# Optimization experiments

Measured on AMD Instinct MI355X. Metric: run time of the kernel, lower is better.

Reference implementation:

```python
import jax, jax.numpy as jnp
import numpy as np

B, T, N, D = 32, 12, 325, 64
H = 4           # geo_num_heads == t_num_heads
HD = D // H     # head_dim = 16
M_SP = 32       # spatial frequency modes (min(32, N//2))
M_T = T // 2    # temporal frequency modes (all low modes)
SCALE = HD ** -0.5


def _lin(x, W):
    # torch nn.Linear (no bias): y = x @ W.T, W: [out, in]
    return jnp.einsum('btnd,ed->btne', x, W)


def _spatial(x, Wq, Wk, Wv, weights_Q, sp_modes):
    # FEDformer-style frequency attention over the node axis N
    q, k, v = _lin(x, Wq), _lin(x, Wk), _lin(x, Wv)          # [B,T,N,D]
    prep = lambda y: y.reshape(B, T, N, H, HD).transpose(0, 1, 3, 4, 2)  # [B,T,H,HD,N]
    qn = prep(q) / jnp.linalg.norm(q)   # global Frobenius norm (torch.norm with no dim)
    kn = prep(k) / jnp.linalg.norm(k)
    vn = prep(v)
    # rfft over nodes, gather selected modes (scatter-into-zeros in torch == gather here
    # since target indices are 0..M-1)
    qf = jnp.fft.rfft(qn, axis=-1)[..., sp_modes]            # [B,T,H,HD,M] c64
    kf = jnp.fft.rfft(kn, axis=-1)[..., sp_modes]
    vf = jnp.fft.rfft(vn, axis=-1)[..., sp_modes]
    M = M_SP
    qg = qf.transpose(0, 1, 2, 4, 3)[:, :, :, :, None, :]    # [B,T,H,M,1,HD]
    wq = jnp.broadcast_to(weights_Q.astype(jnp.complex64), (B, T, H, M, M - 1, HD))
    q_cat = jnp.concatenate([qg, wq], axis=4)                # [B,T,H,M,M,HD]
    kg = kf.transpose(0, 1, 2, 4, 3)[:, :, :, None, :, :]    # [B,T,H,1,M,HD]
    att = kg * jnp.conj(q_cat) * SCALE                       # [B,T,H,M,M,HD] c64
    att = jax.nn.softmax(jnp.abs(att), axis=-2).astype(jnp.complex64)
    att = att.transpose(0, 1, 2, 3, 5, 4)                    # [B,T,H,M,HD,M]
    vg = vf[:, :, :, None, :, :]                             # [B,T,H,1,HD,M]
    out = (vg * jnp.conj(att)).mean(axis=3)                  # [B,T,H,HD,M]
    out_ft = jnp.zeros((B, T, H, HD, N // 2 + 1), jnp.complex64).at[..., sp_modes].set(out)
    y = jnp.fft.irfft(out_ft, n=N, axis=-1)                  # [B,T,H,HD,N]
    return y.transpose(0, 1, 4, 2, 3).reshape(B, T, N, D)


def _temporal(x, Wq, Wk, Wv, weights_Q_t, t_modes):
    # frequency attention over the time axis T with causal (tril) mask.
    # NOTE: torch reshapes the [B,T,N,D] buffer directly as [B,N,T,H,HD] (raw view),
    # so we replicate that exact buffer reinterpretation.
    q, k, v = _lin(x, Wq), _lin(x, Wk), _lin(x, Wv)
    prep = lambda y: y.reshape(B, N, T, H, HD).transpose(0, 1, 3, 4, 2)  # [B,N,H,HD,T]
    qn = prep(q); kn = prep(k); vn = prep(v)
    qn = qn / jnp.linalg.norm(qn)
    kn = kn / jnp.linalg.norm(kn)
    qf = jnp.fft.rfft(qn, axis=-1)[..., t_modes]             # [B,N,H,HD,Mt]
    kf = jnp.fft.rfft(kn, axis=-1)[..., t_modes]
    vf = jnp.fft.rfft(vn, axis=-1)[..., t_modes]
    Mt = M_T
    qg = qf.transpose(0, 1, 2, 4, 3)[:, :, :, :, None, :]    # [B,N,H,Mt,1,HD]
    wq = jnp.broadcast_to(weights_Q_t.astype(jnp.complex64), (B, N, H, Mt, Mt - 1, HD))
    q_cat = jnp.concatenate([qg, wq], axis=4)                # [B,N,H,Mt,Mt,HD]
    kg = kf.transpose(0, 1, 2, 4, 3)[:, :, :, :, None, :]    # [B,N,H,Mt,1,HD] (unsqueeze(4) in torch)
    att = kg * jnp.conj(q_cat) * SCALE                       # [B,N,H,Mt,Mt,HD]
    att = att.transpose(0, 1, 2, 5, 3, 4)                    # [B,N,H,HD,Mt,Mt]
    mask = jnp.tril(jnp.ones((Mt, Mt), jnp.float32))
    att = att * mask                                         # zero above diagonal
    attw = jax.nn.softmax(jnp.abs(att), axis=-1).astype(jnp.complex64)
    vg = vf[..., None]                                       # [B,N,H,HD,Mt,1]
    out = (vg * jnp.conj(attw)).mean(axis=-1)                # [B,N,H,HD,Mt]
    out_ft = jnp.zeros((B, N, H, HD, T // 2 + 1), jnp.complex64).at[..., t_modes].set(out)
    y = jnp.fft.irfft(out_ft, n=T, axis=-1)                  # [B,N,H,HD,T]
    return y.transpose(0, 4, 1, 2, 3).reshape(B, T, N, D)


def _gcn(x, adj, W_fc1, W_mlp, b_mlp):
    a = adj / jnp.sum(adj, axis=1, keepdims=True)            # row-normalized
    agg = jnp.einsum('btkd,nk->btnd', x, a)
    h = jnp.einsum('btnd,ed->btne', agg, W_fc1)              # fc1 (no bias)
    return jnp.einsum('btnd,ed->btne', h, W_mlp) + b_mlp     # mlp (bias)


def _forward(x, adj, Wq_geo, Wk_geo, Wv_geo, Wq_t, Wk_t, Wv_t,
             W_fc1, W_mlp, b_mlp, weights_Q, weights_Q_t, sp_modes, t_modes):
    gcn_out = _gcn(x, adj, W_fc1, W_mlp, b_mlp)
    sp_x = _spatial(x, Wq_geo, Wk_geo, Wv_geo, weights_Q, sp_modes)
    te_x = _temporal(x, Wq_t, Wk_t, Wv_t, weights_Q_t, t_modes)
    return gcn_out + sp_x + te_x   # proj_drop is identity (p=0)


def setup_inputs() -> dict:
    key = jax.random.key(0)
    ks = jax.random.split(key, 13)
    w = lambda k, s: jax.random.normal(k, s, dtype=jnp.float32) * 0.05
    rng = np.random.default_rng(0)
    sp_modes = np.sort(rng.permutation(N // 2)[:M_SP]).astype(np.int32)
    t_modes = np.arange(M_T, dtype=np.int32)  # modes_T == T//2 selects all low modes
    return {
        'x': jax.random.normal(ks[0], (B, T, N, D), dtype=jnp.float32),
        'adj': jax.random.uniform(ks[1], (N, N), dtype=jnp.float32),
        'Wq_geo': w(ks[2], (D, D)), 'Wk_geo': w(ks[3], (D, D)), 'Wv_geo': w(ks[4], (D, D)),
        'Wq_t': w(ks[5], (D, D)), 'Wk_t': w(ks[6], (D, D)), 'Wv_t': w(ks[7], (D, D)),
        'W_fc1': w(ks[8], (D, D)), 'W_mlp': w(ks[9], (D, D)), 'b_mlp': w(ks[10], (D,)),
        'weights_Q': jax.random.normal(ks[11], (M_SP, M_SP - 1, HD), dtype=jnp.float32),
        'weights_Q_t': jax.random.normal(ks[12], (M_T, M_T - 1, HD), dtype=jnp.float32),
        'sp_modes': jnp.asarray(sp_modes),
        't_modes': jnp.asarray(t_modes),
    }


def reference(x, adj, Wq_geo, Wk_geo, Wv_geo, Wq_t, Wk_t, Wv_t,
              W_fc1, W_mlp, b_mlp, weights_Q, weights_Q_t, sp_modes, t_modes):
    return _forward(x, adj, Wq_geo, Wk_geo, Wv_geo, Wq_t, Wk_t, Wv_t,
                    W_fc1, W_mlp, b_mlp, weights_Q, weights_Q_t, sp_modes, t_modes)
```

## Files before the change

kernel.cpp:

```cpp
#include <hip/hip_runtime.h>


typedef unsigned short u16;
typedef short short8 __attribute__((ext_vector_type(8)));
typedef float floatx4 __attribute__((ext_vector_type(4)));

__device__ __forceinline__ u16 f2bf(float f) {
  union { float fp; unsigned int u; } v; v.fp = f;
  unsigned int x = v.u;
  x += 0x7FFF + ((x >> 16) & 1);
  return (u16)(x >> 16);
}

constexpr size_t OFF_NPART = 4096;
constexpr size_t OFF_WQA  = 8208;
constexpr size_t OFF_ANB  = 24080;
constexpr size_t OFF_TB   = 81280;
constexpr size_t OFF_WVTB = 92544;
constexpr size_t OFF_WBB  = 94592;
constexpr size_t OFF_T2   = 102080;
constexpr size_t OFF_OFT  = 112480;
constexpr size_t OFF_XCT  = 898912;
constexpr size_t OFF_XA   = 13211488;
constexpr size_t OFF_WSPB = OFF_XA + 8192;

__global__ __launch_bounds__(256) void k_prep(const float* __restrict__ adj,
                                              const float* __restrict__ Wmlp,
                                              const float* __restrict__ Wfc1,
                                              const float* __restrict__ wQ,
                                              const float* __restrict__ Wvt,
                                              const float* __restrict__ Wq,
                                              const float* __restrict__ Wk,
                                              const float* __restrict__ Wv,
                                              const int* __restrict__ sp_modes,
                                              float* __restrict__ ws) {
  __shared__ float red[256];
  const int tid = threadIdx.x;
  const int blk = blockIdx.x;
  u16* WBBu = (u16*)(ws + OFF_WBB);
  if (blk == 0) {
    for (int o = tid; o < 4096; o += 256) {
      int g = o >> 6, dd = o & 63;
      float s = 0.f;
      for (int e = 0; e < 64; ++e)
        s = fmaf(Wmlp[g * 64 + e], Wfc1[e * 64 + dd], s);
      WBBu[o] = f2bf(s);
    }
  } else if (blk < 9) {
    for (int i = (blk - 1) * 256 + tid; i < 15872; i += 2048)
      ws[OFF_WQA + i] = fabsf(wQ[i]);
  } else if (blk < 334) {
    const int n = blk - 9;
    float p = 0.f;
    for (int k = tid; k < 325; k += 256) p += adj[n * 325 + k];
    red[tid] = p;
    __syncthreads();
    for (int s2 = 128; s2 > 0; s2 >>= 1) {
      if (tid < s2) red[tid] += red[tid + s2];
      __syncthreads();
    }
    const float inv = 1.f / red[0];
    u16* ANB = (u16*)(ws + OFF_ANB);
    for (int k = tid; k < 352; k += 256)
      ANB[(size_t)n * 352 + k] = (k < 325) ? f2bf(adj[n * 325 + k] * inv) : (u16)0;
  } else if (blk < 366) {
    const int j = blk - 334;
    const int f = sp_modes[j];
    const float wgt = (f == 0) ? 1.f : 2.f;
    u16* T2B = (u16*)(ws + OFF_T2);
    u16* TB = (u16*)(ws + OFF_TB);
    const int row_re = 8 * (j >> 2) + (j & 3);
    const int row_im = row_re + 4;
    for (int n = tid; n < 352; n += 256) {
      float c = 0.f, s = 0.f;
      if (n < 325) {
        int mm = (f * n) % 325;
        float th = 6.283185307179586f * (float)mm * (1.f / 325.f);
        c = cosf(th);
        s = sinf(th);
      }
      TB[(size_t)row_re * 352 + n] = f2bf(c);
      TB[(size_t)row_im * 352 + n] = f2bf(-s);
      if (n < 325) {
        T2B[(size_t)n * 64 + 2 * j] = f2bf(wgt * (1.f / 325.f) * c);
        T2B[(size_t)n * 64 + 2 * j + 1] = f2bf(-wgt * (1.f / 325.f) * s);
      }
    }
  } else if (blk == 366) {
    for (int i = tid; i < 8192; i += 256) {
      const int r = i >> 6, e = i & 63;
      const float* src = (r < 64) ? Wq : Wk;
      WBBu[4096 + i] = f2bf(src[(size_t)(r & 63) * 64 + e]);
    }
  } else if (blk == 367) {
    u16* WSPBu = (u16*)(ws + OFF_WSPB);
    for (int i = tid; i < 12288; i += 256) {
      const int r = i >> 6, e = i & 63;
      const float* src = (r < 64) ? Wq : (r < 128) ? Wk : Wv;
      WSPBu[i] = f2bf(src[(size_t)(r & 63) * 64 + e]);
    }
  } else if (blk == 368) {
    u16* WVTBu = (u16*)(ws + OFF_WVTB);
    for (int i = tid; i < 4096; i += 256) WVTBu[i] = f2bf(Wvt[i]);
  } else {
    const int idx = (blk - 369) * 256 + tid;
    u16* p = (u16*)(ws + OFF_XCT) + (size_t)(idx >> 6) * 22528 + (size_t)(idx & 63) * 352;
    for (int c = 325; c < 352; ++c) p[c] = 0;
  }
}

__global__ __launch_bounds__(512, 3) void k_linear2(const float* __restrict__ x,
                                                    float* __restrict__ ws) {
  __shared__ __align__(16) u16 XA[128 * 72];
  __shared__ float reds[16];
  const int tid = threadIdx.x;
  const int wv = tid >> 6, lane = tid & 63, lc = lane & 15, quad = lane >> 4;
  const size_t base = (size_t)blockIdx.x * 128;
  const u16* WBBu = (const u16*)(ws + OFF_WBB);

  for (int i = tid; i < 2048; i += 512) {
    const int row = i >> 4, e0 = (i & 15) * 4;
    const float4 v = *(const float4*)(x + (base + row) * 64 + e0);
    u16* dst = &XA[row * 72 + e0];
    dst[0] = f2bf(v.x); dst[1] = f2bf(v.y); dst[2] = f2bf(v.z); dst[3] = f2bf(v.w);
  }
  __syncthreads();

  floatx4 acc[12] = {};
#pragma unroll
  for (int kc = 0; kc < 2; ++kc) {
    const short8 af = *(const short8*)&XA[(16 * wv + lc) * 72 + kc * 32 + quad * 8];
#pragma unroll
    for (int ni = 0; ni < 12; ++ni) {
      const short8 bf_ = *(const short8*)&WBBu[(ni * 16 + lc) * 64 + kc * 32 + quad * 8];
      acc[ni] = __builtin_amdgcn_mfma_f32_16x16x32_bf16(af, bf_, acc[ni], 0, 0, 0);
    }
  }

  float sq = 0.f, sk = 0.f;
#pragma unroll
  for (int reg = 0; reg < 4; ++reg) {
#pragma unroll
    for (int ni = 0; ni < 4; ++ni) {
      const float v = acc[4 + ni][reg];
      sq = fmaf(v, v, sq);
    }
#pragma unroll
    for (int ni = 0; ni < 4; ++ni) {
      const float v = acc[8 + ni][reg];
      sk = fmaf(v, v, sk);
    }
  }
  for (int off = 32; off > 0; off >>= 1) {
    sq += __shfl_down(sq, off);
    sk += __shfl_down(sk, off);
  }
  if (lane == 0) { reds[wv] = sq; reds[8 + wv] = sk; }
  __syncthreads();
  if (tid == 0) {
    const float a = reds[0] + reds[1] + reds[2] + reds[3] +
                    reds[4] + reds[5] + reds[6] + reds[7];
    const float b = reds[8] + reds[9] + reds[10] + reds[11] +
                    reds[12] + reds[13] + reds[14] + reds[15];
    *(float2*)(ws + OFF_NPART + 2 * (size_t)blockIdx.x) = make_float2(a, b);
  }

  u16* xcT = XA;
#pragma unroll
  for (int ni = 0; ni < 4; ++ni)
#pragma unroll
    for (int reg = 0; reg < 4; ++reg)
      xcT[(ni * 16 + lc) * 132 + 16 * wv + quad * 4 + reg] = f2bf(acc[ni][reg]);
  __syncthreads();
  u16* XCT = (u16*)(ws + OFF_XCT);
  for (int i = tid; i < 8192; i += 512) {
    const int d = i >> 7, r = i & 127;
    const unsigned int row = (unsigned int)(base + r);
    const unsigned int bt = row / 325u;
    const unsigned int n = row - bt * 325u;
    XCT[(size_t)bt * 22528 + (size_t)d * 352 + n] = xcT[d * 132 + r];
  }
}

__global__ __launch_bounds__(256) void k_spatial3(const float* __restrict__ x,
                                                  float* __restrict__ ws) {
  __shared__ __align__(16) float smem[10256];
  const int tid = threadIdx.x;
  const int bt = blockIdx.x;
  const int lane = tid & 63, wv = tid >> 6;
  const int lc = lane & 15, quad = lane >> 4;

  {
    float psq = 0.f, psk = 0.f;
    for (int p = tid; p < 975; p += 256) {
      const float2 v = *(const float2*)(ws + OFF_NPART + 2 * (size_t)p);
      psq += v.x; psk += v.y;
    }
    for (int off = 32; off > 0; off >>= 1) {
      psq += __shfl_down(psq, off);
      psk += __shfl_down(psk, off);
    }
    if (lane == 0) { smem[10240 + wv] = psq; smem[10248 + wv] = psk; }
  }

  u16* Bt = (u16*)smem;
  u16* xfl2 = (u16*)smem + 5120;
  const u16* TB = (const u16*)(ws + OFF_TB);
  const u16* WSPBu = (const u16*)(ws + OFF_WSPB);
  const float* xb = x + (size_t)bt * 20800;
  const int br = tid & 31, be0 = (tid >> 5) * 8;

  auto stageB = [&](int kc, u16* dst) {
    const int k0 = kc * 32;
    float v[8];
    if (k0 + br < 325) {
      const float* src = xb + (size_t)(k0 + br) * 64 + be0;
      *(float4*)v = *(const float4*)src;
      *(float4*)(v + 4) = *(const float4*)(src + 4);
    } else {
#pragma unroll
      for (int u = 0; u < 8; ++u) v[u] = 0.f;
    }
#pragma unroll
    for (int u = 0; u < 8; ++u) dst[(be0 + u) * 40 + br] = f2bf(v[u]);
  };

  floatx4 accA[4] = {};
  stageB(0, Bt);
  __syncthreads();
  for (int kc = 0; kc < 11; ++kc) {
    u16* cur = Bt + (kc & 1) * 2560;
    if (kc < 10) stageB(kc + 1, Bt + ((kc + 1) & 1) * 2560);
    const short8 af = *(const short8*)&TB[(size_t)(16 * wv + lc) * 352 + kc * 32 + quad * 8];
#pragma unroll
    for (int t = 0; t < 4; ++t) {
      const short8 bf_ = *(const short8*)&cur[(t * 16 + lc) * 40 + quad * 8];
      accA[t] = __builtin_amdgcn_mfma_f32_16x16x32_bf16(af, bf_, accA[t], 0, 0, 0);
    }
    __syncthreads();
  }

#pragma unroll
  for (int t = 0; t < 4; ++t)
#pragma unroll
    for (int r = 0; r < 4; ++r)
      xfl2[(t >> 1) * 2560 + (16 * wv + quad * 4 + r) * 40 + (t & 1) * 16 + lc] =
          f2bf(accA[t][r]);
  __syncthreads();

  floatx4 acc2[12] = {};
#pragma unroll
  for (int kc2 = 0; kc2 < 2; ++kc2) {
    const short8 af2 = *(const short8*)&xfl2[kc2 * 2560 + (16 * wv + lc) * 40 + quad * 8];
#pragma unroll
    for (int t = 0; t < 12; ++t) {
      const short8 bf2 = *(const short8*)&WSPBu[(t * 16 + lc) * 64 + kc2 * 32 + quad * 8];
      acc2[t] = __builtin_amdgcn_mfma_f32_16x16x32_bf16(af2, bf2, acc2[t], 0, 0, 0);
    }
  }
  __syncthreads();

  float* sq_q = smem;
  float* sq_k = smem + 2048;
  float* vfre = smem + 4096;
  float* vfim = smem + 6144;
  float* wbar = smem + 8192;
  for (int i = tid; i < 2048; i += 256) wbar[i] = 0.f;
  {
    const int fb = 8 * wv + ((quad >= 2) ? 4 : 0);
    const int isim = quad & 1;
#pragma unroll
    for (int t = 0; t < 12; ++t) {
      const int mat = t >> 2;
      const int d = (t & 3) * 16 + lc;
#pragma unroll
      for (int r = 0; r < 4; ++r) {
        const float v = acc2[t][r];
        if (mat == 2) {
          if (isim) vfim[(fb + r) * 64 + d] = v;
          else vfre[(fb + r) * 64 + d] = v;
        } else {
          const float s2 = v * v + __shfl_xor(v * v, 16);
          if (!isim) {
            if (mat == 0) sq_q[(fb + r) * 64 + d] = s2;
            else sq_k[(fb + r) * 64 + d] = s2;
          }
        }
      }
    }
  }
  __syncthreads();
  float nqs = 0.f, nks = 0.f;
#pragma unroll
  for (int w = 0; w < 4; ++w) { nqs += smem[10240 + w]; nks += smem[10248 + w]; }
  const float inv_nq = rsqrtf(nqs);
  const float inv_nk = rsqrtf(nks);
  for (int i = tid; i < 2048; i += 256)
    sq_k[i] = 0.25f * inv_nk * sqrtf(sq_k[i]);
  __syncthreads();
  {
    const int d = tid & 63, fb2 = tid >> 6, hd = d & 15;
    const float* wqa = ws + OFF_WQA;
    float wacc[32];
#pragma unroll
    for (int j = 0; j < 32; ++j) wacc[j] = 0.f;
    for (int r8 = 0; r8 < 8; ++r8) {
      const int m = fb2 + (r8 << 2);
      const float aq = inv_nq * sqrtf(sq_q[m * 64 + d]);
      float sv[32];
      float mx = -1e30f;
#pragma unroll
      for (int j = 0; j < 32; ++j) {
        const float a = (j == 0) ? aq : wqa[(m * 31 + (j - 1)) * 16 + hd];
        const float s = sq_k[j * 64 + d] * a;
        sv[j] = s;
        mx = fmaxf(mx, s);
      }
      float sum = 0.f;
#pragma unroll
      for (int j = 0; j < 32; ++j) {
        const float ev = __expf(sv[j] - mx);
        sv[j] = ev;
        sum += ev;
      }
      const float sc = 0.03125f / sum;
#pragma unroll
      for (int j = 0; j < 32; ++j) wacc[j] += sv[j] * sc;
    }
#pragma unroll
    for (int j = 0; j < 32; ++j) atomicAdd(&wbar[j * 64 + d], wacc[j]);
  }
  __syncthreads();
  unsigned int* OFTu = (unsigned int*)(ws + OFF_OFT) + (size_t)bt * 2048;
  for (int i2 = tid; i2 < 2048; i2 += 256) {
    const int d = i2 >> 5, j = i2 & 31;
    const float w = wbar[j * 64 + d];
    const unsigned int lo = f2bf(vfre[j * 64 + d] * w);
    const unsigned int hi = f2bf(vfim[j * 64 + d] * w);
    OFTu[i2] = lo | (hi << 16);
  }
}

__global__ __launch_bounds__(256) void k_xa(const float* __restrict__ x,
                                            float* __restrict__ ws) {
  const int idx = blockIdx.x * 256 + threadIdx.x;
  if (idx >= 32 * 325 * 16) return;
  const int dq = idx & 15;
  const int n = (idx >> 4) % 325;
  const int b = idx / (16 * 325);
  const float* xp = x + ((size_t)b * 3900 + (size_t)n * 12) * 64 + dq * 4;
  float4 s = make_float4(0.f, 0.f, 0.f, 0.f);
  float sign = 1.f;
  for (int k = 0; k < 12; ++k) {
    const float4 v = *(const float4*)(xp + (size_t)k * 64);
    s.x += sign * v.x; s.y += sign * v.y; s.z += sign * v.z; s.w += sign * v.w;
    sign = -sign;
  }
  *(float4*)(ws + OFF_XA + ((size_t)b * 325 + n) * 64 + dq * 4) = s;
}

__global__ __launch_bounds__(256) void k_final2(const float* __restrict__ x,
                                                const float* __restrict__ bmlp,
                                                float* __restrict__ ws,
                                                float* __restrict__ out) {
  const int tid = threadIdx.x;
  const int bt = blockIdx.x / 3, mc = blockIdx.x % 3;
  const int m0 = mc * 128;
  const int wave = tid >> 6, lane = tid & 63;
  const int quad = lane >> 4, lc = lane & 15;

  const u16* ANB = (const u16*)(ws + OFF_ANB);
  const u16* T2B = (const u16*)(ws + OFF_T2);
  const u16* XCT = (const u16*)(ws + OFF_XCT) + (size_t)bt * 22528;
  const u16* OFT = (const u16*)(ws + OFF_OFT) + (size_t)bt * 4096;
  const u16* WVTBu = (const u16*)(ws + OFF_WVTB);

  const int b = bt / 12, t = bt - b * 12;
  const float sgn12 = ((t & 1) ? -1.f : 1.f) * (1.f / 12.f);

  floatx4 acc[2][4] = {};

#pragma unroll
  for (int c13 = 0; c13 < 13; ++c13) {
    const bool gcn = (c13 < 11);
    const u16* Asrc = gcn ? ANB : T2B;
    const int astr = gcn ? 352 : 64;
    const int acol = gcn ? c13 * 32 : (c13 - 11) * 32;
    const u16* Bsrc = gcn ? XCT : OFT;
    const int bstr = gcn ? 352 : 64;
    short8 af[2], bf_[4];
#pragma unroll
    for (int mi = 0; mi < 2; ++mi) {
      const int gr = m0 + wave * 32 + mi * 16 + lc;
      short8 a = {};
      if (gr < 325)
        a = *(const short8*)&Asrc[(size_t)gr * astr + acol + quad * 8];
      af[mi] = a;
    }
#pragma unroll
    for (int ni = 0; ni < 4; ++ni)
      bf_[ni] = *(const short8*)&Bsrc[(size_t)(ni * 16 + lc) * bstr + acol + quad * 8];
#pragma unroll
    for (int mi = 0; mi < 2; ++mi)
#pragma unroll
      for (int ni = 0; ni < 4; ++ni)
        acc[mi][ni] = __builtin_amdgcn_mfma_f32_16x16x32_bf16(
            af[mi], bf_[ni], acc[mi][ni], 0, 0, 0);
  }

#pragma unroll
  for (int kc = 0; kc < 2; ++kc) {
    const int k0 = kc * 32 + quad * 8;
    short8 af[2];
#pragma unroll
    for (int mi = 0; mi < 2; ++mi) {
      const int nr = m0 + wave * 32 + mi * 16 + lc;
      short8 a = {};
      if (nr < 325) {
        const float* xp = x + ((size_t)b * 3900 + (size_t)nr * 12 + t) * 64 + k0;
        const float* xap = ws + OFF_XA + ((size_t)b * 325 + nr) * 64 + k0;
        float xv[8], av[8];
        *(float4*)xv = *(const float4*)xp;
        *(float4*)(xv + 4) = *(const float4*)(xp + 4);
        *(float4*)av = *(const float4*)xap;
        *(float4*)(av + 4) = *(const float4*)(xap + 4);
#pragma unroll
        for (int u = 0; u < 8; ++u)
          a[u] = (short)f2bf((xv[u] - sgn12 * av[u]) * (1.f / 6.f));
      }
      af[mi] = a;
    }
#pragma unroll
    for (int ni = 0; ni < 4; ++ni) {
      const short8 bf_ = *(const short8*)&WVTBu[(size_t)(ni * 16 + lc) * 64 + k0];
#pragma unroll
      for (int mi = 0; mi < 2; ++mi)
        acc[mi][ni] = __builtin_amdgcn_mfma_f32_16x16x32_bf16(
            af[mi], bf_, acc[mi][ni], 0, 0, 0);
    }
  }

#pragma unroll
  for (int ni = 0; ni < 4; ++ni) {
    const int d = ni * 16 + lc;
    const float bias = bmlp[d];
#pragma unroll
    for (int mi = 0; mi < 2; ++mi) {
#pragma unroll
      for (int reg = 0; reg < 4; ++reg) {
        const int n = m0 + wave * 32 + mi * 16 + quad * 4 + reg;
        if (n >= 325) continue;
        out[((size_t)bt * 325 + n) * 64 + d] = acc[mi][ni][reg] + bias;
      }
    }
  }
}

extern "C" void kernel_launch(void* const* d_in, const int* in_sizes, int n_in,
                              void* d_out, int out_size, void* d_ws, size_t ws_size,
                              hipStream_t stream) {
  const float* x = (const float*)d_in[0];
  const float* adj = (const float*)d_in[1];
  const float* Wq_g = (const float*)d_in[2];
  const float* Wk_g = (const float*)d_in[3];
  const float* Wv_g = (const float*)d_in[4];
  const float* Wv_t = (const float*)d_in[7];
  const float* Wfc1 = (const float*)d_in[8];
  const float* Wmlp = (const float*)d_in[9];
  const float* bmlp = (const float*)d_in[10];
  const float* wQ = (const float*)d_in[11];
  const int* sp_modes = (const int*)d_in[13];
  float* ws = (float*)d_ws;
  float* out = (float*)d_out;

  (void)in_sizes; (void)n_in; (void)out_size; (void)ws_size;

  k_prep<<<465, 256, 0, stream>>>(adj, Wmlp, Wfc1, wQ, Wv_t, Wq_g, Wk_g, Wv_g,
                                  sp_modes, ws);
  k_linear2<<<975, 512, 0, stream>>>(x, ws);
  k_spatial3<<<384, 256, 0, stream>>>(x, ws);
  k_xa<<<650, 256, 0, stream>>>(x, ws);
  k_final2<<<1152, 256, 0, stream>>>(x, bmlp, ws, out);
}
```

Baseline: 255.2 us.

## Stage whole node slab into LDS upfront, drop per-chunk double-buffer syncs

The k_spatial3 kernel now loads the entire per-(b,t) x slab (352 padded nodes × 64 dims) into shared memory as bf16 in three batched load groups. It then runs all 11 MFMA k-chunks with no barrier between them, replacing the double-buffered per-chunk staging that synced on every iteration. Issuing more global loads together aims to raise memory-level parallelism and cut synchronization overhead. In exchange, shared memory per block grows from about 41KB to 51KB, which may lower occupancy, and the later buffers are shifted to avoid overlapping with the reused region.

```diff
diff --git a/kernel.cpp b/kernel.cpp
--- a/kernel.cpp
+++ b/kernel.cpp
@@ -184,11 +184,12 @@
 
 __global__ __launch_bounds__(256) void k_spatial3(const float* __restrict__ x,
                                                   float* __restrict__ ws) {
-  __shared__ __align__(16) float smem[10256];
+  __shared__ __align__(16) float smem[12816];
   const int tid = threadIdx.x;
   const int bt = blockIdx.x;
   const int lane = tid & 63, wv = tid >> 6;
   const int lc = lane & 15, quad = lane >> 4;
+  u16* XBu = (u16*)smem;
 
   {
     float psq = 0.f, psk = 0.f;
@@ -200,46 +201,57 @@
       psq += __shfl_down(psq, off);
       psk += __shfl_down(psk, off);
     }
-    if (lane == 0) { smem[10240 + wv] = psq; smem[10248 + wv] = psk; }
-  }
-
-  u16* Bt = (u16*)smem;
-  u16* xfl2 = (u16*)smem + 5120;
+    if (lane == 0) { smem[12800 + wv] = psq; smem[12808 + wv] = psk; }
+  }
+
   const u16* TB = (const u16*)(ws + OFF_TB);
   const u16* WSPBu = (const u16*)(ws + OFF_WSPB);
   const float* xb = x + (size_t)bt * 20800;
   const int br = tid & 31, be0 = (tid >> 5) * 8;
 
-  auto stageB = [&](int kc, u16* dst) {
-    const int k0 = kc * 32;
-    float v[8];
-    if (k0 + br < 325) {
-      const float* src = xb + (size_t)(k0 + br) * 64 + be0;
-      *(float4*)v = *(const float4*)src;
-      *(float4*)(v + 4) = *(const float4*)(src + 4);
-    } else {
-#pragma unroll
-      for (int u = 0; u < 8; ++u) v[u] = 0.f;
-    }
-#pragma unroll
-    for (int u = 0; u < 8; ++u) dst[(be0 + u) * 40 + br] = f2bf(v[u]);
-  };
+  {
+    float va[4][8];
+#pragma unroll
+    for (int g = 0; g < 3; ++g) {
+      const int nkc = (g < 2) ? 4 : 3;
+#pragma unroll
+      for (int u = 0; u < 4; ++u) {
+        if (u >= nkc) break;
+        const int k0 = (g * 4 + u) * 32;
+        if (k0 + br < 325) {
+          const float* src = xb + (size_t)(k0 + br) * 64 + be0;
+          *(float4*)&va[u][0] = *(const float4*)src;
+          *(float4*)&va[u][4] = *(const float4*)(src + 4);
+        } else {
+#pragma unroll
+          for (int w = 0; w < 8; ++w) va[u][w] = 0.f;
+        }
+      }
+#pragma unroll
+      for (int u = 0; u < 4; ++u) {
+        if (u >= nkc) break;
+        const int k0 = (g * 4 + u) * 32;
+#pragma unroll
+        for (int w = 0; w < 8; ++w)
+          XBu[(be0 + w) * 360 + k0 + br] = f2bf(va[u][w]);
+      }
+    }
+  }
+  __syncthreads();
 
   floatx4 accA[4] = {};
-  stageB(0, Bt);
-  __syncthreads();
+#pragma unroll
   for (int kc = 0; kc < 11; ++kc) {
-    u16* cur = Bt + (kc & 1) * 2560;
-    if (kc < 10) stageB(kc + 1, Bt + ((kc + 1) & 1) * 2560);
     const short8 af = *(const short8*)&TB[(size_t)(16 * wv + lc) * 352 + kc * 32 + quad * 8];
 #pragma unroll
     for (int t = 0; t < 4; ++t) {
-      const short8 bf_ = *(const short8*)&cur[(t * 16 + lc) * 40 + quad * 8];
+      const short8 bf_ = *(const short8*)&XBu[(t * 16 + lc) * 360 + kc * 32 + quad * 8];
       accA[t] = __builtin_amdgcn_mfma_f32_16x16x32_bf16(af, bf_, accA[t], 0, 0, 0);
     }
-    __syncthreads();
-  }
-
+  }
+  __syncthreads();
+
+  u16* xfl2 = XBu;
 #pragma unroll
   for (int t = 0; t < 4; ++t)
 #pragma unroll
@@ -260,11 +272,11 @@
   }
   __syncthreads();
 
-  float* sq_q = smem;
-  float* sq_k = smem + 2048;
-  float* vfre = smem + 4096;
-  float* vfim = smem + 6144;
-  float* wbar = smem + 8192;
+  float* sq_q = smem + 2560;
+  float* sq_k = smem + 4608;
+  float* vfre = smem + 6656;
+  float* vfim = smem + 8704;
+  float* wbar = smem + 10752;
   for (int i = tid; i < 2048; i += 256) wbar[i] = 0.f;
   {
     const int fb = 8 * wv + ((quad >= 2) ? 4 : 0);
@@ -292,7 +304,7 @@
   __syncthreads();
   float nqs = 0.f, nks = 0.f;
 #pragma unroll
-  for (int w = 0; w < 4; ++w) { nqs += smem[10240 + w]; nks += smem[10248 + w]; }
+  for (int w = 0; w < 4; ++w) { nqs += smem[12800 + w]; nks += smem[12808 + w]; }
   const float inv_nq = rsqrtf(nqs);
   const float inv_nk = rsqrtf(nks);
   for (int i = tid; i < 2048; i += 256)
```

New measurement: 253.9 us. Within noise of the previous version (-0.5%).
